# Optimization experiments

Measured on AMD Instinct MI355X. Metric: run time of the kernel, lower is better.

## Reference

```python
import jax, jax.numpy as jnp
import numpy as np

HIDDEN = 1024
HEADS = 16
HEAD_DIM = HIDDEN // HEADS
B, S = 4, 2048


def setup_inputs() -> dict:
    key = jax.random.key(0)
    ks = jax.random.split(key, 12)
    d = {
        "query": jax.random.normal(ks[0], (B, S, HIDDEN), jnp.float32),
        "key": jax.random.normal(ks[1], (B, S, HIDDEN), jnp.float32),
        "value": jax.random.normal(ks[2], (B, S, HIDDEN), jnp.float32),
        "relative_time": jax.random.normal(ks[3], (B, 1, S, S), jnp.float32),
        # causal boolean mask (True = attend), matches masked_fill_(~mask)
        "attn_mask": jnp.broadcast_to(jnp.tril(jnp.ones((S, S), bool)), (B, S, S)),
    }
    scale = 1.0 / np.sqrt(HIDDEN)
    for i, name in enumerate(["q", "k", "v", "out"]):
        d[f"W{name}"] = jax.random.normal(ks[4 + 2 * i], (HIDDEN, HIDDEN), jnp.float32) * scale
        d[f"b{name}"] = jax.random.normal(ks[5 + 2 * i], (HIDDEN,), jnp.float32) * 0.01
    return d


def reference(query, key, value, relative_time, attn_mask,
              Wq, bq, Wk, bk, Wv, bv, Wout, bout):
    Bsz, Slen, _ = query.shape
    # linear projections (torch Linear: x @ W^T + b)
    Q = query @ Wq.T + bq
    K = key @ Wk.T + bk
    V = value @ Wv.T + bv
    # [B, H, S, Dh]
    Q = Q.reshape(Bsz, Slen, HEADS, HEAD_DIM).transpose(0, 2, 1, 3)
    K = K.reshape(Bsz, Slen, HEADS, HEAD_DIM).transpose(0, 2, 1, 3)
    V = V.reshape(Bsz, Slen, HEADS, HEAD_DIM).transpose(0, 2, 1, 3)

    scale = HEAD_DIM ** (-0.5)
    # scores: [B, H, S, S]; bias added BEFORE scaling, as in the original
    scores = jnp.einsum("bhqd,bhkd->bhqk", Q, K)
    scores = (scores + relative_time) * scale
    scores = jnp.where(attn_mask[:, None, :, :], scores, -jnp.inf)
    attn = jax.nn.softmax(scores, axis=-1)
    attn = jnp.nan_to_num(attn, nan=0.0)  # fully-masked rows -> 0
    # dropout: inference mode (training=False) -> identity
    out = jnp.einsum("bhqk,bhkd->bhqd", attn, V)
    out = out.transpose(0, 2, 1, 3).reshape(Bsz, Slen, HIDDEN)
    return out @ Wout.T + bout
```

## Files before the change

### kernel.cpp

```cpp
#include <hip/hip_runtime.h>


#define SEQ 2048
#define NH 16
#define DH 64
#define HID 1024
#define QSCALE 0.18033688011112f

typedef short bf16x8 __attribute__((ext_vector_type(8)));
typedef float f32x4  __attribute__((ext_vector_type(4)));
typedef unsigned short u16;
typedef unsigned short u16x4 __attribute__((ext_vector_type(4)));
typedef unsigned short u16x8 __attribute__((ext_vector_type(8)));

__device__ __forceinline__ float b2f(u16 u) {
    union { unsigned i; float f; } x; x.i = ((unsigned)u) << 16; return x.f;
}
__device__ __forceinline__ u16 f2b(float f) {
    union { float f; unsigned i; } x; x.f = f;
    unsigned r = x.i + 0x7fffu + ((x.i >> 16) & 1u);
    return (u16)(r >> 16);
}

typedef const __attribute__((address_space(1))) unsigned int guint;
typedef __attribute__((address_space(3))) unsigned int luint;
__device__ __forceinline__ void gload_lds16(const u16* g, u16* l) {
    __builtin_amdgcn_global_load_lds((guint*)g, (luint*)l, 16, 0, 0);
}

__global__ __launch_bounds__(256) void cvt_bf16_kernel(
    const float* __restrict__ in, u16* __restrict__ out, int n8)
{
    int i = blockIdx.x * 256 + threadIdx.x;
    const int stride = gridDim.x * 256;
    for (; i < n8; i += stride) {
        f32x4 a = *(const f32x4*)(in + (size_t)i * 8);
        f32x4 b = *(const f32x4*)(in + (size_t)i * 8 + 4);
        u16x8 o;
#pragma unroll
        for (int j = 0; j < 4; ++j) { o[j] = f2b(a[j]); o[j + 4] = f2b(b[j]); }
        *(u16x8*)(out + (size_t)i * 8) = o;
    }
}

__global__ __launch_bounds__(256) void rel_perm_kernel(
    const float* __restrict__ rel, u16* __restrict__ out)
{
    __shared__ u16 pl[4096];
    const int t   = threadIdx.x;
    const int blk = blockIdx.x;
    const int b   = blk >> 10;
    const int qc  = (blk >> 5) & 31;
    const int kc  = blk & 31;
    const int qloc  = t >> 2;
    const int kloc0 = (t & 3) << 4;

    const float* src = rel + ((size_t)b * SEQ + qc * 64 + qloc) * SEQ + kc * 64 + kloc0;
    const int qt   = qloc >> 4;
    const int quad = (qloc >> 2) & 3;
    const int g    = qloc & 3;
    const int nt   = t & 3;
    u16* dst = pl + qt * 1024 + quad * 256 + nt * 4 + g;
#pragma unroll
    for (int c = 0; c < 4; ++c) {
        f32x4 x = *(const f32x4*)(src + c * 4);
#pragma unroll
        for (int j = 0; j < 4; ++j)
            dst[(c * 4 + j) * 16] = f2b(x[j] * QSCALE);
    }
    __syncthreads();
    const size_t obase = (((size_t)b * 128 + qc * 4) * 32 + kc) * 1024;
#pragma unroll
    for (int q2 = 0; q2 < 4; ++q2)
        *(u16x4*)(out + obase + (size_t)q2 * 32768 + t * 4) =
            *(const u16x4*)(pl + q2 * 1024 + t * 4);
}

#define GSWZ(R, C) (((R) << 5) + ((((C) ^ (((R) >> 1) & 3))) << 3))

__global__ __launch_bounds__(256) void qkv_proj_kernel(
    const u16* __restrict__ xq, const u16* __restrict__ xk, const u16* __restrict__ xv,
    const u16* __restrict__ wq, const u16* __restrict__ wk, const u16* __restrict__ wv,
    const float* __restrict__ bq, const float* __restrict__ bk, const float* __restrict__ bv,
    u16* __restrict__ Qw, u16* __restrict__ Kw, u16* __restrict__ Vw)
{
    __shared__ __align__(16) u16 As[128 * 32];
    __shared__ __align__(16) u16 Bs[128 * 32];

    const int tid  = threadIdx.x;
    const int w    = tid >> 6;
    const int lane = tid & 63;
    const int l16  = lane & 15;
    const int quad = lane >> 4;

    const int lbid = ((blockIdx.x & 7) * 192) + (blockIdx.x >> 3);
    const int sel = lbid >> 9;
    const int rem = lbid & 511;
    const int tm = rem >> 3, tn = rem & 7;
    const int m0 = tm << 7, n0 = tn << 7;

    const u16* X    = sel == 0 ? xq : (sel == 1 ? xk : xv);
    const u16* W    = sel == 0 ? wq : (sel == 1 ? wk : wv);
    const float* bias = sel == 0 ? bq : (sel == 1 ? bk : bv);

    const int crow = lane >> 2;
    const int csw  = (((lane & 3) ^ ((lane >> 3) & 3)) << 3);

    f32x4 acc[4][4];
    const f32x4 zero = {0.f, 0.f, 0.f, 0.f};
#pragma unroll
    for (int r = 0; r < 4; ++r)
#pragma unroll
        for (int c = 0; c < 4; ++c) acc[r][c] = zero;

    const int wr = (w >> 1) << 6;
    const int wc = (w & 1) << 6;

    for (int k0 = 0; k0 < 1024; k0 += 32) {
#pragma unroll
        for (int c = 0; c < 2; ++c) {
            const int ch  = w + c * 4;
            const int row = ch * 16 + crow;
            gload_lds16(X + (size_t)(m0 + row) * 1024 + k0 + csw, As + ch * 512 + lane * 8);
            gload_lds16(W + (size_t)(n0 + row) * 1024 + k0 + csw, Bs + ch * 512 + lane * 8);
        }
        __syncthreads();
        bf16x8 a[4], b[4];
#pragma unroll
        for (int r = 0; r < 4; ++r) {
            const int R = wr + r * 16 + l16;
            a[r] = *(const bf16x8*)(As + GSWZ(R, quad));
        }
#pragma unroll
        for (int c = 0; c < 4; ++c) {
            const int R = wc + c * 16 + l16;
            b[c] = *(const bf16x8*)(Bs + GSWZ(R, quad));
        }
#pragma unroll
        for (int r = 0; r < 4; ++r)
#pragma unroll
            for (int c = 0; c < 4; ++c)
                acc[r][c] = __builtin_amdgcn_mfma_f32_16x16x32_bf16(a[r], b[c], acc[r][c], 0, 0, 0);
        __syncthreads();
    }

#pragma unroll
    for (int c = 0; c < 4; ++c) {
        const int n = n0 + wc + c * 16 + l16;
        const float bn = bias[n];
        const int h = n >> 6, d = n & 63;
#pragma unroll
        for (int r = 0; r < 4; ++r) {
#pragma unroll
            for (int g = 0; g < 4; ++g) {
                const int m  = m0 + wr + r * 16 + quad * 4 + g;
                const int b_ = m >> 11, s_ = m & 2047;
                const float val = acc[r][c][g] + bn;
                if (sel == 0)
                    Qw[(((size_t)(b_ * 16 + h)) * 2048 + s_) * 64 + d] = f2b(val * QSCALE);
                else if (sel == 1)
                    Kw[(((size_t)(b_ * 16 + h)) * 2048 + s_) * 64 + d] = f2b(val);
                else
                    Vw[(((size_t)(b_ * 16 + h)) * 64 + d) * 2048 + s_] = f2b(val);
            }
        }
    }
}

#define SWZ(R, C) (((R) << 6) + ((((C) ^ ((R) & 7))) << 3))

__global__ __launch_bounds__(512, 4) void attn_kernel(
    const u16* __restrict__ Qb, const u16* __restrict__ Kb,
    const u16* __restrict__ Vb, const u16* __restrict__ relb,
    u16* __restrict__ Ob)
{
    __shared__ __align__(16) u16 lds[25600];
    const int tid  = threadIdx.x;
    const int w    = tid >> 6;
    const int lane = tid & 63;
    const int l16  = lane & 15;
    const int quad = lane >> 4;
    u16* Pl = lds + 16384 + w * 1152;

    const int bh = blockIdx.x & 63;
    const int p  = blockIdx.x >> 6;
    const int b  = bh >> 4, h = bh & 15;

    const u16* Qp = Qb + (size_t)bh * SEQ * DH;
    const u16* Kg = Kb + (size_t)bh * SEQ * DH;
    const u16* Vg = Vb + (size_t)bh * DH * SEQ;

    const int r0 = tid >> 3;
    const int c0 = tid & 7;
    const int o0 = c0 << 3;
    const int sw0 = ((c0 ^ (r0 & 7)) << 3);

    for (int sidx = 0; sidx < 2; ++sidx) {
        const int qb  = sidx ? (15 - p) : p;
        const int q0w = qb * 128 + w * 16;

        bf16x8 qa[2];
#pragma unroll
        for (int ks = 0; ks < 2; ++ks)
            qa[ks] = *(const bf16x8*)(Qp + (size_t)(q0w + l16) * 64 + ks * 32 + quad * 8);

        f32x4 o[4], mrow, lrow;
        const f32x4 zero = {0.f, 0.f, 0.f, 0.f};
        const f32x4 ninf = {-1e30f, -1e30f, -1e30f, -1e30f};
        mrow = ninf; lrow = zero;
#pragma unroll
        for (int dt = 0; dt < 4; ++dt) o[dt] = zero;

        const int ntiles  = qb * 2 + 2;
        const int mytiles = qb * 2 + (w >> 2) + 1;

        const u16* relW = relb + ((size_t)(b * 128 + (q0w >> 4))) * 32768 + (size_t)lane * 16;

        bf16x8 kreg = *(const bf16x8*)(Kg + (size_t)r0 * 64 + o0);
        bf16x8 vreg = *(const bf16x8*)(Vg + (size_t)r0 * 2048 + o0);
        bf16x8 rr0 = *(const bf16x8*)(relW);
        bf16x8 rr1 = *(const bf16x8*)(relW + 8);

        for (int kt = 0; kt < ntiles; ++kt) {
            const int k0 = kt << 6;
            u16* Ksb = lds + ((kt & 1) << 12);
            u16* Vtb = lds + 8192 + ((kt & 1) << 12);
            *(bf16x8*)(Ksb + r0 * 64 + sw0) = kreg;
            *(bf16x8*)(Vtb + r0 * 64 + sw0) = vreg;

            const bool act = kt < mytiles;
            f32x4 s[4];
            if (act) {
#pragma unroll
                for (int nt = 0; nt < 4; ++nt)
#pragma unroll
                    for (int g = 0; g < 4; ++g)
                        s[nt][g] = b2f((u16)((nt < 2 ? rr0 : rr1)[(nt & 1) * 4 + g]));
            }

            const int ktn = (kt + 1 < ntiles) ? kt + 1 : kt;
            const int kn  = ktn << 6;
            kreg = *(const bf16x8*)(Kg + (size_t)(kn + r0) * 64 + o0);
            vreg = *(const bf16x8*)(Vg + (size_t)r0 * 2048 + kn + o0);
            rr0  = *(const bf16x8*)(relW + (size_t)ktn * 1024);
            rr1  = *(const bf16x8*)(relW + (size_t)ktn * 1024 + 8);

            __syncthreads();

            if (act) {
#pragma unroll
                for (int nt = 0; nt < 4; ++nt) {
                    const int R = nt * 16 + l16;
                    bf16x8 kb0 = *(const bf16x8*)(Ksb + SWZ(R, quad));
                    bf16x8 kb1 = *(const bf16x8*)(Ksb + SWZ(R, 4 | quad));
                    s[nt] = __builtin_amdgcn_mfma_f32_16x16x32_bf16(qa[0], kb0, s[nt], 0, 0, 0);
                    s[nt] = __builtin_amdgcn_mfma_f32_16x16x32_bf16(qa[1], kb1, s[nt], 0, 0, 0);
                }
                if (kt == mytiles - 1) {
#pragma unroll
                    for (int nt = 0; nt < 4; ++nt)
#pragma unroll
                        for (int g = 0; g < 4; ++g) {
                            const int q = q0w + quad * 4 + g;
                            const int k = k0 + nt * 16 + l16;
                            if (k > q) s[nt][g] = -1e30f;
                        }
                }
                {
                    f32x4 t;
#pragma unroll
                    for (int g = 0; g < 4; ++g)
                        t[g] = fmaxf(fmaxf(s[0][g], s[1][g]), fmaxf(s[2][g], s[3][g]));
#pragma unroll
                    for (int off = 1; off < 16; off <<= 1)
#pragma unroll
                        for (int g = 0; g < 4; ++g)
                            t[g] = fmaxf(t[g], __shfl_xor(t[g], off, 64));
                    f32x4 mn, alpha;
#pragma unroll
                    for (int g = 0; g < 4; ++g) {
                        mn[g] = fmaxf(mrow[g], t[g]);
                        alpha[g] = __builtin_amdgcn_exp2f(mrow[g] - mn[g]);
                    }
                    mrow = mn;
#pragma unroll
                    for (int dt = 0; dt < 4; ++dt)
#pragma unroll
                        for (int g = 0; g < 4; ++g) o[dt][g] *= alpha[g];
#pragma unroll
                    for (int nt = 0; nt < 4; ++nt)
#pragma unroll
                        for (int g = 0; g < 4; ++g)
                            s[nt][g] = __builtin_amdgcn_exp2f(s[nt][g] - mn[g]);
#pragma unroll
                    for (int g = 0; g < 4; ++g)
                        lrow[g] = lrow[g] * alpha[g]
                                + ((s[0][g] + s[1][g]) + (s[2][g] + s[3][g]));
                }
#pragma unroll
                for (int nt = 0; nt < 4; ++nt)
#pragma unroll
                    for (int g = 0; g < 4; ++g)
                        Pl[(quad * 4 + g) * 72 + nt * 16 + l16] = f2b(s[nt][g]);
                bf16x8 pa[2];
#pragma unroll
                for (int ks = 0; ks < 2; ++ks)
                    pa[ks] = *(const bf16x8*)(Pl + l16 * 72 + ks * 32 + quad * 8);
#pragma unroll
                for (int dt = 0; dt < 4; ++dt) {
                    const int R = dt * 16 + l16;
                    bf16x8 vb0 = *(const bf16x8*)(Vtb + SWZ(R, quad));
                    bf16x8 vb1 = *(const bf16x8*)(Vtb + SWZ(R, 4 | quad));
                    o[dt] = __builtin_amdgcn_mfma_f32_16x16x32_bf16(pa[0], vb0, o[dt], 0, 0, 0);
                    o[dt] = __builtin_amdgcn_mfma_f32_16x16x32_bf16(pa[1], vb1, o[dt], 0, 0, 0);
                }
            }
        }

#pragma unroll
        for (int off = 1; off < 16; off <<= 1)
#pragma unroll
            for (int g = 0; g < 4; ++g)
                lrow[g] += __shfl_xor(lrow[g], off, 64);
        {
            f32x4 linv;
#pragma unroll
            for (int g = 0; g < 4; ++g) linv[g] = 1.0f / lrow[g];
#pragma unroll
            for (int dt = 0; dt < 4; ++dt)
#pragma unroll
                for (int g = 0; g < 4; ++g)
                    Pl[(quad * 4 + g) * 72 + dt * 16 + l16] = f2b(o[dt][g] * linv[g]);
        }
#pragma unroll
        for (int pp = 0; pp < 2; ++pp) {
            const int c = lane + pp * 64;
            const int row = c >> 3, col = (c & 7) << 3;
            bf16x8 t = *(const bf16x8*)(Pl + row * 72 + col);
            *(bf16x8*)(Ob + ((size_t)b * SEQ + q0w + row) * HID + h * DH + col) = t;
        }
    }
}

__global__ __launch_bounds__(256) void out_proj_kernel(
    const u16* __restrict__ X, const u16* __restrict__ W,
    const float* __restrict__ bias, float* __restrict__ out)
{
    __shared__ __align__(16) u16 As[128 * 32];
    __shared__ __align__(16) u16 Bs[128 * 32];

    const int tid  = threadIdx.x;
    const int w    = tid >> 6;
    const int lane = tid & 63;
    const int l16  = lane & 15;
    const int quad = lane >> 4;

    const int lbid = ((blockIdx.x & 7) * 64) + (blockIdx.x >> 3);
    const int tm = lbid >> 3, tn = lbid & 7;
    const int m0 = tm << 7, n0 = tn << 7;

    const int crow = lane >> 2;
    const int csw  = (((lane & 3) ^ ((lane >> 3) & 3)) << 3);

    f32x4 acc[4][4];
    const f32x4 zero = {0.f, 0.f, 0.f, 0.f};
#pragma unroll
    for (int r = 0; r < 4; ++r)
#pragma unroll
        for (int c = 0; c < 4; ++c) acc[r][c] = zero;

    const int wr = (w >> 1) << 6;
    const int wc = (w & 1) << 6;

    for (int k0 = 0; k0 < 1024; k0 += 32) {
#pragma unroll
        for (int c = 0; c < 2; ++c) {
            const int ch  = w + c * 4;
            const int row = ch * 16 + crow;
            gload_lds16(X + (size_t)(m0 + row) * 1024 + k0 + csw, As + ch * 512 + lane * 8);
            gload_lds16(W + (size_t)(n0 + row) * 1024 + k0 + csw, Bs + ch * 512 + lane * 8);
        }
        __syncthreads();
        bf16x8 a[4], b[4];
#pragma unroll
        for (int r = 0; r < 4; ++r) {
            const int R = wr + r * 16 + l16;
            a[r] = *(const bf16x8*)(As + GSWZ(R, quad));
        }
#pragma unroll
        for (int c = 0; c < 4; ++c) {
            const int R = wc + c * 16 + l16;
            b[c] = *(const bf16x8*)(Bs + GSWZ(R, quad));
        }
#pragma unroll
        for (int r = 0; r < 4; ++r)
#pragma unroll
            for (int c = 0; c < 4; ++c)
                acc[r][c] = __builtin_amdgcn_mfma_f32_16x16x32_bf16(a[r], b[c], acc[r][c], 0, 0, 0);
        __syncthreads();
    }

#pragma unroll
    for (int c = 0; c < 4; ++c) {
        const int n = n0 + wc + c * 16 + l16;
        const float bn = bias[n];
#pragma unroll
        for (int r = 0; r < 4; ++r) {
#pragma unroll
            for (int g = 0; g < 4; ++g) {
                const int m = m0 + wr + r * 16 + quad * 4 + g;
                out[(size_t)m * 1024 + n] = acc[r][c][g] + bn;
            }
        }
    }
}

extern "C" void kernel_launch(void* const* d_in, const int* in_sizes, int n_in,
                              void* d_out, int out_size, void* d_ws, size_t ws_size,
                              hipStream_t stream)
{
    const float* q   = (const float*)d_in[0];
    const float* k   = (const float*)d_in[1];
    const float* v   = (const float*)d_in[2];
    const float* rel = (const float*)d_in[3];
    const float* wq = (const float*)d_in[5];  const float* bq = (const float*)d_in[6];
    const float* wk = (const float*)d_in[7];  const float* bk = (const float*)d_in[8];
    const float* wv = (const float*)d_in[9];  const float* bv = (const float*)d_in[10];
    const float* wo = (const float*)d_in[11]; const float* bo = (const float*)d_in[12];

    u16* ws = (u16*)d_ws;
    u16* Qw   = ws;
    u16* Kw   = ws + 8388608ULL;
    u16* Vw   = ws + 16777216ULL;
    u16* Ow   = ws + 25165824ULL;
    u16* relb = ws + 33554432ULL;

    u16* Xqb = Ow;
    u16* Xkb = relb;
    u16* Xvb = relb + 8388608ULL;
    u16* Wqb = (u16*)d_out;
    u16* Wkb = Wqb + 1048576ULL;
    u16* Wvb = Wqb + 2097152ULL;
    u16* Wob = Qw;

    cvt_bf16_kernel<<<1024, 256, 0, stream>>>(q, Xqb, 1048576);
    cvt_bf16_kernel<<<1024, 256, 0, stream>>>(k, Xkb, 1048576);
    cvt_bf16_kernel<<<1024, 256, 0, stream>>>(v, Xvb, 1048576);
    cvt_bf16_kernel<<<512, 256, 0, stream>>>(wq, Wqb, 131072);
    cvt_bf16_kernel<<<512, 256, 0, stream>>>(wk, Wkb, 131072);
    cvt_bf16_kernel<<<512, 256, 0, stream>>>(wv, Wvb, 131072);

    qkv_proj_kernel<<<1536, 256, 0, stream>>>(Xqb, Xkb, Xvb, Wqb, Wkb, Wvb,
                                              bq, bk, bv, Qw, Kw, Vw);
    rel_perm_kernel<<<4096, 256, 0, stream>>>(rel, relb);
    attn_kernel<<<512, 512, 0, stream>>>(Qw, Kw, Vw, relb, Ow);
    cvt_bf16_kernel<<<512, 256, 0, stream>>>(wo, Wob, 131072);
    out_proj_kernel<<<512, 256, 0, stream>>>(Ow, Wob, bo, (float*)d_out);
}
```

Measured before the change: 452.8 us.

## Double-buffer LDS in projection GEMMs and stage QKV epilogue for coalesced stores

Both projection GEMMs now use a two-slot LDS ring, issuing the next k-tile's global-to-LDS loads before computing on the current one, so load latency overlaps MFMA work. The QKV epilogue writes results into LDS first and then emits 16-byte vector stores, including a transposed write for V, instead of scattered 2-byte stores. This targets memory latency stalls and uncoalesced writes, at the cost of doubled LDS per block and possible occupancy loss. Correctness of the overlap depends on the async loads into the next buffer completing before the barrier, which the code relies on implicitly.

Result: faster. 435.8 us (-3.8%).

```diff
diff --git a/kernel.cpp b/kernel.cpp
--- a/kernel.cpp
+++ b/kernel.cpp
@@ -84,8 +84,7 @@
     const float* __restrict__ bq, const float* __restrict__ bk, const float* __restrict__ bv,
     u16* __restrict__ Qw, u16* __restrict__ Kw, u16* __restrict__ Vw)
 {
-    __shared__ __align__(16) u16 As[128 * 32];
-    __shared__ __align__(16) u16 Bs[128 * 32];
+    __shared__ __align__(16) u16 sm[16384];
 
     const int tid  = threadIdx.x;
     const int w    = tid >> 6;
@@ -116,25 +115,41 @@
     const int wr = (w >> 1) << 6;
     const int wc = (w & 1) << 6;
 
-    for (int k0 = 0; k0 < 1024; k0 += 32) {
+    {
 #pragma unroll
         for (int c = 0; c < 2; ++c) {
             const int ch  = w + c * 4;
             const int row = ch * 16 + crow;
-            gload_lds16(X + (size_t)(m0 + row) * 1024 + k0 + csw, As + ch * 512 + lane * 8);
-            gload_lds16(W + (size_t)(n0 + row) * 1024 + k0 + csw, Bs + ch * 512 + lane * 8);
+            gload_lds16(X + (size_t)(m0 + row) * 1024 + csw, sm + ch * 512 + lane * 8);
+            gload_lds16(W + (size_t)(n0 + row) * 1024 + csw, sm + 8192 + ch * 512 + lane * 8);
         }
         __syncthreads();
+    }
+    for (int t = 0; t < 32; ++t) {
+        if (t < 31) {
+            const int kn = (t + 1) << 5;
+            u16* a = sm + (((t + 1) & 1) << 12);
+            u16* bL = sm + 8192 + (((t + 1) & 1) << 12);
+#pragma unroll
+            for (int c = 0; c < 2; ++c) {
+                const int ch  = w + c * 4;
+                const int row = ch * 16 + crow;
+                gload_lds16(X + (size_t)(m0 + row) * 1024 + kn + csw, a + ch * 512 + lane * 8);
+                gload_lds16(W + (size_t)(n0 + row) * 1024 + kn + csw, bL + ch * 512 + lane * 8);
+            }
+        }
+        const u16* As_ = sm + ((t & 1) << 12);
+        const u16* Bs_ = sm + 8192 + ((t & 1) << 12);
         bf16x8 a[4], b[4];
 #pragma unroll
         for (int r = 0; r < 4; ++r) {
             const int R = wr + r * 16 + l16;
-            a[r] = *(const bf16x8*)(As + GSWZ(R, quad));
+            a[r] = *(const bf16x8*)(As_ + GSWZ(R, quad));
         }
 #pragma unroll
         for (int c = 0; c < 4; ++c) {
             const int R = wc + c * 16 + l16;
-            b[c] = *(const bf16x8*)(Bs + GSWZ(R, quad));
+            b[c] = *(const bf16x8*)(Bs_ + GSWZ(R, quad));
         }
 #pragma unroll
         for (int r = 0; r < 4; ++r)
@@ -144,25 +159,55 @@
         __syncthreads();
     }
 
-#pragma unroll
-    for (int c = 0; c < 4; ++c) {
-        const int n = n0 + wc + c * 16 + l16;
-        const float bn = bias[n];
-        const int h = n >> 6, d = n & 63;
-#pragma unroll
-        for (int r = 0; r < 4; ++r) {
-#pragma unroll
-            for (int g = 0; g < 4; ++g) {
-                const int m  = m0 + wr + r * 16 + quad * 4 + g;
-                const int b_ = m >> 11, s_ = m & 2047;
-                const float val = acc[r][c][g] + bn;
-                if (sel == 0)
-                    Qw[(((size_t)(b_ * 16 + h)) * 2048 + s_) * 64 + d] = f2b(val * QSCALE);
-                else if (sel == 1)
-                    Kw[(((size_t)(b_ * 16 + h)) * 2048 + s_) * 64 + d] = f2b(val);
-                else
-                    Vw[(((size_t)(b_ * 16 + h)) * 64 + d) * 2048 + s_] = f2b(val);
-            }
+    const int b_ = m0 >> 11;
+    const int s0 = m0 & 2047;
+    const int h0 = n0 >> 6;
+    const float qsc = (sel == 0) ? QSCALE : 1.0f;
+
+    if (sel < 2) {
+#pragma unroll
+        for (int c = 0; c < 4; ++c) {
+            const int nloc = wc + c * 16 + l16;
+            const float bn = bias[n0 + nloc];
+#pragma unroll
+            for (int r = 0; r < 4; ++r)
+#pragma unroll
+                for (int g = 0; g < 4; ++g) {
+                    const int mloc = wr + r * 16 + quad * 4 + g;
+                    sm[mloc * 128 + nloc] = f2b((acc[r][c][g] + bn) * qsc);
+                }
+        }
+        __syncthreads();
+        u16* dst = (sel == 0) ? Qw : Kw;
+#pragma unroll
+        for (int i = 0; i < 8; ++i) {
+            const int ci = i * 256 + tid;
+            const int mloc = ci >> 4, cl = ci & 15;
+            u16x8 vch = *(const u16x8*)(sm + mloc * 128 + cl * 8);
+            *(u16x8*)(dst + (((size_t)(b_ * 16 + h0 + (cl >> 3))) * 2048 + s0 + mloc) * 64
+                          + (cl & 7) * 8) = vch;
+        }
+    } else {
+#pragma unroll
+        for (int c = 0; c < 4; ++c) {
+            const int nloc = wc + c * 16 + l16;
+            const float bn = bias[n0 + nloc];
+#pragma unroll
+            for (int r = 0; r < 4; ++r)
+#pragma unroll
+                for (int g = 0; g < 4; ++g) {
+                    const int mloc = wr + r * 16 + quad * 4 + g;
+                    sm[nloc * 128 + mloc] = f2b(acc[r][c][g] + bn);
+                }
+        }
+        __syncthreads();
+#pragma unroll
+        for (int i = 0; i < 8; ++i) {
+            const int ci = i * 256 + tid;
+            const int nloc = ci >> 4, cl = ci & 15;
+            u16x8 vch = *(const u16x8*)(sm + nloc * 128 + cl * 8);
+            *(u16x8*)(Vw + (((size_t)(b_ * 16 + h0 + (nloc >> 6))) * 64 + (nloc & 63)) * 2048
+                          + s0 + cl * 8) = vch;
         }
     }
 }
@@ -346,8 +391,7 @@
     const u16* __restrict__ X, const u16* __restrict__ W,
     const float* __restrict__ bias, float* __restrict__ out)
 {
-    __shared__ __align__(16) u16 As[128 * 32];
-    __shared__ __align__(16) u16 Bs[128 * 32];
+    __shared__ __align__(16) u16 sm[16384];
 
     const int tid  = threadIdx.x;
     const int w    = tid >> 6;
@@ -372,25 +416,41 @@
     const int wr = (w >> 1) << 6;
     const int wc = (w & 1) << 6;
 
-    for (int k0 = 0; k0 < 1024; k0 += 32) {
+    {
 #pragma unroll
         for (int c = 0; c < 2; ++c) {
             const int ch  = w + c * 4;
             const int row = ch * 16 + crow;
-            gload_lds16(X + (size_t)(m0 + row) * 1024 + k0 + csw, As + ch * 512 + lane * 8);
-            gload_lds16(W + (size_t)(n0 + row) * 1024 + k0 + csw, Bs + ch * 512 + lane * 8);
+            gload_lds16(X + (size_t)(m0 + row) * 1024 + csw, sm + ch * 512 + lane * 8);
+            gload_lds16(W + (size_t)(n0 + row) * 1024 + csw, sm + 8192 + ch * 512 + lane * 8);
         }
         __syncthreads();
+    }
+    for (int t = 0; t < 32; ++t) {
+        if (t < 31) {
+            const int kn = (t + 1) << 5;
+            u16* a = sm + (((t + 1) & 1) << 12);
+            u16* bL = sm + 8192 + (((t + 1) & 1) << 12);
+#pragma unroll
+            for (int c = 0; c < 2; ++c) {
+                const int ch  = w + c * 4;
+                const int row = ch * 16 + crow;
+                gload_lds16(X + (size_t)(m0 + row) * 1024 + kn + csw, a + ch * 512 + lane * 8);
+                gload_lds16(W + (size_t)(n0 + row) * 1024 + kn + csw, bL + ch * 512 + lane * 8);
+            }
+        }
+        const u16* As_ = sm + ((t & 1) << 12);
+        const u16* Bs_ = sm + 8192 + ((t & 1) << 12);
         bf16x8 a[4], b[4];
 #pragma unroll
         for (int r = 0; r < 4; ++r) {
             const int R = wr + r * 16 + l16;
-            a[r] = *(const bf16x8*)(As + GSWZ(R, quad));
+            a[r] = *(const bf16x8*)(As_ + GSWZ(R, quad));
         }
 #pragma unroll
         for (int c = 0; c < 4; ++c) {
             const int R = wc + c * 16 + l16;
-            b[c] = *(const bf16x8*)(Bs + GSWZ(R, quad));
+            b[c] = *(const bf16x8*)(Bs_ + GSWZ(R, quad));
         }
 #pragma unroll
         for (int r = 0; r < 4; ++r)
```
